# Kernel tuning notes

Hardware: AMD Instinct MI355X
Metric: run time of the kernel (lower is better)

Reference implementation:

```python
import jax, jax.numpy as jnp
import numpy as np

B, N, C = 2, 2048, 1024
H = 16
HD = C // H  # 64
SCALE = HD ** -0.5


def setup_inputs() -> dict:
    key = jax.random.key(0)
    ks = jax.random.split(key, 5)
    x = jax.random.normal(ks[0], (B, N, C), dtype=jnp.float32)
    # Linear params stored as [in, out] so y = x @ W + b (same math as torch x @ W.T + b)
    w_qkv = jax.random.normal(ks[1], (C, 3 * C), dtype=jnp.float32) * (C ** -0.5)
    b_qkv = jax.random.normal(ks[2], (3 * C,), dtype=jnp.float32) * 0.02
    w_proj = jax.random.normal(ks[3], (C, C), dtype=jnp.float32) * (C ** -0.5)
    b_proj = jax.random.normal(ks[4], (C,), dtype=jnp.float32) * 0.02
    return {"x": x, "w_qkv": w_qkv, "b_qkv": b_qkv, "w_proj": w_proj, "b_proj": b_proj}


def reference(x, w_qkv, b_qkv, w_proj, b_proj):
    # qkv projection: [B,N,3C] -> [3,B,H,N,HD]
    qkv = (x @ w_qkv + b_qkv).reshape(B, N, 3, H, HD)
    qkv = jnp.transpose(qkv, (2, 0, 3, 1, 4))
    q, k, v = qkv[0], qkv[1], qkv[2]
    # scaled dot-product attention, full [B,H,N,N] scores (faithful to source)
    attn = jnp.einsum('bhnd,bhmd->bhnm', q, k) * SCALE
    attn = jax.nn.softmax(attn, axis=-1)
    out = jnp.einsum('bhnm,bhmd->bhnd', attn, v)  # [B,H,N,HD]
    out = jnp.transpose(out, (0, 2, 1, 3)).reshape(B, N, C)
    return out @ w_proj + b_proj
```

## Files before the change

### kernel.cpp

```cpp
#include <hip/hip_runtime.h>


typedef __attribute__((ext_vector_type(4))) float f32x4;
typedef __attribute__((ext_vector_type(16))) float f32x16;
typedef __attribute__((ext_vector_type(8))) short bf16x8;
typedef __attribute__((ext_vector_type(8))) unsigned short u16x8;
typedef __attribute__((ext_vector_type(4))) unsigned short u16x4;
typedef __attribute__((ext_vector_type(2))) int i32x2;
typedef __attribute__((ext_vector_type(4))) int i32x4;

#define MFMA16 __builtin_amdgcn_mfma_f32_16x16x32_bf16
#define MFMA32 __builtin_amdgcn_mfma_f32_32x32x16_bf16
#define MEMFENCE asm volatile("" ::: "memory")
#define BARRIER() do { MEMFENCE; __builtin_amdgcn_s_barrier(); MEMFENCE; } while (0)

__device__ __forceinline__ unsigned short f2bf(float f) {
  unsigned int u = __float_as_uint(f);
  u += 0x7fffu + ((u >> 16) & 1u);
  return (unsigned short)(u >> 16);
}
__device__ __forceinline__ float bf2f(unsigned short h) {
  return __uint_as_float(((unsigned int)h) << 16);
}
__device__ __forceinline__ void gll16(const unsigned short* g, unsigned short* l) {
  __builtin_amdgcn_global_load_lds(
      (__attribute__((address_space(1))) void*)g,
      (__attribute__((address_space(3))) void*)l, 16, 0, 0);
}

__global__ __launch_bounds__(256) void prep_w_hi_kernel(
    const float* __restrict__ w, unsigned short* __restrict__ hi, int K, int N) {
  __shared__ float tile[64][65];
  const int k0 = blockIdx.x * 64, n0 = blockIdx.y * 64;
  const int tid = threadIdx.x;
  {
    const int r = tid >> 4, c = (tid & 15) * 4;
#pragma unroll
    for (int i = 0; i < 4; ++i) {
      const float4 v = *(const float4*)&w[(size_t)(k0 + r + i * 16) * N + n0 + c];
      tile[r + i * 16][c + 0] = v.x; tile[r + i * 16][c + 1] = v.y;
      tile[r + i * 16][c + 2] = v.z; tile[r + i * 16][c + 3] = v.w;
    }
  }
  __syncthreads();
  const int rn = tid >> 2, cb = (tid & 3) * 16;
  u16x8 h8[2];
#pragma unroll
  for (int j = 0; j < 16; ++j)
    h8[j >> 3][j & 7] = f2bf(tile[cb + j][rn]);
  const size_t o = (size_t)(n0 + rn) * K + k0 + cb;
  *(u16x8*)&hi[o] = h8[0]; *(u16x8*)&hi[o + 8] = h8[1];
}

__global__ __launch_bounds__(256) void cast_x_kernel(
    const float* __restrict__ x, unsigned short* __restrict__ hi) {
  const size_t i = ((size_t)blockIdx.x * 256 + threadIdx.x) * 4;
  const float4 v = *(const float4*)&x[i];
  u16x4 h;
  h[0] = f2bf(v.x); h[1] = f2bf(v.y); h[2] = f2bf(v.z); h[3] = f2bf(v.w);
  *(u16x4*)&hi[i] = h;
}

__global__ __launch_bounds__(256) void gemm_qkv_kernel(
    const unsigned short* __restrict__ Ahg, const unsigned short* __restrict__ Bhg,
    const float* __restrict__ bias,
    unsigned short* __restrict__ q_hi, unsigned short* __restrict__ k_hi,
    unsigned short* __restrict__ vt_hi) {
  __shared__ unsigned short Ah_s[3][128 * 32], Bh_s[3][128 * 32];
  const int tid = threadIdx.x;
  const int n0 = blockIdx.x * 128, m0 = blockIdx.y * 128;
  const int w = tid >> 6, lane = tid & 63;
  const int wm = (w >> 1) * 64, wn = (w & 1) * 64;
  const int lr = lane & 15, lg = lane >> 4;
  const int rr = lane >> 2, sl = lane & 3;
  const int r0 = w * 32 + rr;
  const int c0 = (sl ^ ((r0 >> 1) & 3)) * 8;
  const size_t a0 = (size_t)(m0 + r0) * 1024 + c0;
  const size_t a1 = (size_t)(m0 + r0 + 16) * 1024 + c0;
  const size_t b0 = (size_t)(n0 + r0) * 1024 + c0;
  const size_t b1 = (size_t)(n0 + r0 + 16) * 1024 + c0;
  const int wo = w * 1024;

#define GSTAGE(BUF, KO) do {                                          \
    gll16(&Ahg[a0 + (KO)], &Ah_s[BUF][wo]);                           \
    gll16(&Ahg[a1 + (KO)], &Ah_s[BUF][wo + 512]);                     \
    gll16(&Bhg[b0 + (KO)], &Bh_s[BUF][wo]);                           \
    gll16(&Bhg[b1 + (KO)], &Bh_s[BUF][wo + 512]);                     \
  } while (0)

  f32x4 acc[4][4] = {};
  GSTAGE(0, 0);
  GSTAGE(1, 32);
  int cur = 0;
  for (int t = 0; t < 32; ++t) {
    if (t < 31) asm volatile("s_waitcnt vmcnt(4)" ::: "memory");
    else        asm volatile("s_waitcnt vmcnt(0)" ::: "memory");
    __builtin_amdgcn_sched_barrier(0);
    BARRIER();
    if (t < 30) GSTAGE((cur + 2) % 3, (t + 2) * 32);
    bf16x8 afh[4], bfh[4];
#pragma unroll
    for (int i = 0; i < 4; ++i) {
      const int rA = wm + i * 16 + lr;
      const int oA = rA * 64 + ((lg * 16) ^ (((rA >> 1) & 3) << 4));
      afh[i] = *(const bf16x8*)((const char*)&Ah_s[cur][0] + oA);
      const int rB = wn + i * 16 + lr;
      const int oB = rB * 64 + ((lg * 16) ^ (((rB >> 1) & 3) << 4));
      bfh[i] = *(const bf16x8*)((const char*)&Bh_s[cur][0] + oB);
    }
#pragma unroll
    for (int i = 0; i < 4; ++i)
#pragma unroll
      for (int j = 0; j < 4; ++j)
        acc[i][j] = MFMA16(afh[i], bfh[j], acc[i][j], 0, 0, 0);
    cur = (cur + 1) % 3;
  }
#undef GSTAGE
#pragma unroll
  for (int j = 0; j < 4; ++j) {
    const int colg = n0 + wn + j * 16 + lr;
    const float bv = bias[colg];
    const int s = colg >> 10;
    const int c = colg & 1023;
    const int hh = c >> 6, d = c & 63;
    const float scl = (s == 0) ? 0.18033688011112042f : 1.0f;
#pragma unroll
    for (int i = 0; i < 4; ++i) {
      const int mg = m0 + wm + i * 16 + lg * 4;
      const int b = mg >> 11, nt = mg & 2047;
      if (s < 2) {
        unsigned short* dst = (s == 0) ? q_hi : k_hi;
        const size_t base = ((size_t)(b * 16 + hh) * 2048 + nt) * 64 + d;
#pragma unroll
        for (int r = 0; r < 4; ++r)
          dst[base + (size_t)r * 64] = f2bf((acc[i][j][r] + bv) * scl);
      } else {
        const size_t base = ((size_t)(b * 16 + hh) * 64 + d) * 2048 + nt;
        u16x4 hv;
#pragma unroll
        for (int r = 0; r < 4; ++r) hv[r] = f2bf(acc[i][j][r] + bv);
        *(u16x4*)&vt_hi[base] = hv;
      }
    }
  }
}

__global__ __launch_bounds__(256, 2) void attn_kernel(
    const unsigned short* __restrict__ q_hi, const unsigned short* __restrict__ k_hi,
    const unsigned short* __restrict__ vt_hi,
    unsigned short* __restrict__ ao_hi) {
  __shared__ unsigned short Kh_s[2][128 * 64];
  __shared__ unsigned short Vh_s[2][64 * 128];
  __shared__ float ls_s[4][32];
  const int tid = threadIdx.x;
  const int w = tid >> 6, lane = tid & 63;
  const int l31 = lane & 31, hi = lane >> 5;
  const int bid = blockIdx.x;
  const int bh = (bid & 7) * 4 + ((bid >> 3) & 3);
  const int qb = bid >> 5;
  const int qwave = qb * 128 + w * 32;

  bf16x8 qfh[4];
  {
    const size_t qrow = ((size_t)bh * 2048 + qwave + l31) * 64;
#pragma unroll
    for (int dc = 0; dc < 4; ++dc)
      qfh[dc] = *(const bf16x8*)&q_hi[qrow + dc * 16 + hi * 8];
  }

  const int krr = lane >> 3;
  const int kslot = (lane & 7) ^ krr;
  const int vrr = lane >> 4;
  const size_t kpan = (size_t)bh * 2048 * 64;
  const size_t vpan = (size_t)bh * 64 * 2048;

#define STAGE(BUF, T) do {                                                   \
    const int kvb_ = (T) * 128;                                              \
    _Pragma("unroll") for (int j = 0; j < 4; ++j) {                          \
      const int ch = 4 * w + j;                                              \
      gll16(&k_hi[kpan + (size_t)(kvb_ + ch * 8 + krr) * 64 + kslot * 8],    \
            &Kh_s[BUF][ch * 512]);                                           \
      const int vrow_ = ch * 4 + vrr;                                        \
      const int vslot_ = (lane & 15) ^ (vrow_ & 7);                          \
      gll16(&vt_hi[vpan + (size_t)vrow_ * 2048 + kvb_ + vslot_ * 8],         \
            &Vh_s[BUF][ch * 512]);                                           \
    } } while (0)

  f32x16 oacc[2] = {};
  float lsp = 0.f;

  STAGE(0, 0);
  int cur = 0;
  for (int t = 0; t < 16; ++t) {
    asm volatile("s_waitcnt vmcnt(0)" ::: "memory");
    __builtin_amdgcn_sched_barrier(0);
    BARRIER();
    if (t < 15) STAGE(cur ^ 1, t + 1);
    const char* Kb = (const char*)&Kh_s[cur][0];
    const char* Vb = (const char*)&Vh_s[cur][0];
#pragma unroll
    for (int s32 = 0; s32 < 4; ++s32) {
      f32x16 sv = {};
      const int krow = s32 * 32 + l31;
      const int kb = krow * 128;
      const int sx = (krow & 7) << 4;
#pragma unroll
      for (int dc = 0; dc < 4; ++dc) {
        const bf16x8 ah = *(const bf16x8*)(Kb + kb + ((dc * 32 + hi * 16) ^ sx));
        sv = MFMA32(ah, qfh[dc], sv, 0, 0, 0);
      }
      float p[16];
#pragma unroll
      for (int r = 0; r < 16; ++r) p[r] = __builtin_amdgcn_exp2f(sv[r]);
      lsp += ((p[0] + p[1]) + (p[2] + p[3])) + ((p[4] + p[5]) + (p[6] + p[7])) +
             (((p[8] + p[9]) + (p[10] + p[11])) + ((p[12] + p[13]) + (p[14] + p[15])));
      unsigned int W[8];
#pragma unroll
      for (int i = 0; i < 8; ++i)
        asm("v_cvt_pk_bf16_f32 %0, %1, %2" : "=v"(W[i]) : "v"(p[2 * i]), "v"(p[2 * i + 1]));
      const i32x2 s02 = __builtin_amdgcn_permlane32_swap((int)W[0], (int)W[2], false, false);
      const i32x2 s13 = __builtin_amdgcn_permlane32_swap((int)W[1], (int)W[3], false, false);
      const i32x2 s46 = __builtin_amdgcn_permlane32_swap((int)W[4], (int)W[6], false, false);
      const i32x2 s57 = __builtin_amdgcn_permlane32_swap((int)W[5], (int)W[7], false, false);
      union { i32x4 i; bf16x8 h; } pa0, pa1;
      pa0.i[0] = s02[0]; pa0.i[1] = s13[0]; pa0.i[2] = s02[1]; pa0.i[3] = s13[1];
      pa1.i[0] = s46[0]; pa1.i[1] = s57[0]; pa1.i[2] = s46[1]; pa1.i[3] = s57[1];
#pragma unroll
      for (int dc = 0; dc < 2; ++dc) {
        const int vrow = dc * 32 + l31;
        const int vb = vrow * 256;
        const int vsx = (vrow & 7) << 4;
#pragma unroll
        for (int kc = 0; kc < 2; ++kc) {
          const int off = (s32 * 64 + kc * 32 + hi * 16) ^ vsx;
          const bf16x8 vh = *(const bf16x8*)(Vb + vb + off);
          const bf16x8 pf = kc ? pa1.h : pa0.h;
          oacc[dc] = MFMA32(pf, vh, oacc[dc], 0, 0, 0);
        }
      }
    }
    cur ^= 1;
  }
#undef STAGE

  {
    const i32x2 sw = __builtin_amdgcn_permlane32_swap(
        __float_as_int(lsp), __float_as_int(lsp), false, false);
    const float lst = __int_as_float(sw[0]) + __int_as_float(sw[1]);
    if (lane < 32) ls_s[w][lane] = lst;
  }
  asm volatile("s_waitcnt lgkmcnt(0)" ::: "memory");
  __builtin_amdgcn_sched_barrier(0);

  const int b = bh >> 4, hh = bh & 15;
#pragma unroll
  for (int r = 0; r < 16; ++r) {
    const int qr = (r & 3) + 8 * (r >> 2) + 4 * hi;
    const float inv = 1.0f / ls_s[w][qr];
    const size_t rowa = ((size_t)b * 2048 + qwave + qr) * 1024 + hh * 64 + l31;
#pragma unroll
    for (int dc = 0; dc < 2; ++dc)
      ao_hi[rowa + dc * 32] = f2bf(oacc[dc][r] * inv);
  }
}

__global__ __launch_bounds__(256) void gemm_proj_kernel(
    const unsigned short* __restrict__ Ahg, const unsigned short* __restrict__ Bhg,
    const float* __restrict__ bias, float* __restrict__ out) {
  __shared__ unsigned short Ah_s[3][64 * 32], Bh_s[3][128 * 32];
  const int tid = threadIdx.x;
  const int n0 = blockIdx.x * 128, m0 = blockIdx.y * 64;
  const int w = tid >> 6, lane = tid & 63;
  const int wm = (w >> 1) * 32, wn = (w & 1) * 64;
  const int lr = lane & 15, lg = lane >> 4;
  const int rla = lane >> 2, sl = lane & 3;
  const int rowA = w * 16 + rla;
  const int colA = (sl ^ ((rowA >> 1) & 3)) * 8;
  const size_t aoff = (size_t)(m0 + rowA) * 1024 + colA;
  const int rowB = w * 32 + rla;
  const int colB = (sl ^ ((rowB >> 1) & 3)) * 8;
  const size_t boff0 = (size_t)(n0 + rowB) * 1024 + colB;
  const size_t boff1 = boff0 + (size_t)16 * 1024;
  const int adst = w * 512, bdst = w * 1024;

#define GSTAGE(BUF, KO) do {                                          \
    gll16(&Ahg[aoff + (KO)], &Ah_s[BUF][adst]);                       \
    gll16(&Bhg[boff0 + (KO)], &Bh_s[BUF][bdst]);                      \
    gll16(&Bhg[boff1 + (KO)], &Bh_s[BUF][bdst + 512]);                \
  } while (0)

  f32x4 acc[2][4] = {};
  GSTAGE(0, 0);
  GSTAGE(1, 32);
  int cur = 0;
  for (int t = 0; t < 32; ++t) {
    if (t < 31) asm volatile("s_waitcnt vmcnt(3)" ::: "memory");
    else        asm volatile("s_waitcnt vmcnt(0)" ::: "memory");
    __builtin_amdgcn_sched_barrier(0);
    BARRIER();
    if (t < 30) GSTAGE((cur + 2) % 3, (t + 2) * 32);
    bf16x8 afh[2], bfh[4];
#pragma unroll
    for (int i = 0; i < 2; ++i) {
      const int rA = wm + i * 16 + lr;
      const int oA = rA * 64 + ((lg * 16) ^ (((rA >> 1) & 3) << 4));
      afh[i] = *(const bf16x8*)((const char*)&Ah_s[cur][0] + oA);
    }
#pragma unroll
    for (int j = 0; j < 4; ++j) {
      const int rB = wn + j * 16 + lr;
      const int oB = rB * 64 + ((lg * 16) ^ (((rB >> 1) & 3) << 4));
      bfh[j] = *(const bf16x8*)((const char*)&Bh_s[cur][0] + oB);
    }
#pragma unroll
    for (int i = 0; i < 2; ++i)
#pragma unroll
      for (int j = 0; j < 4; ++j)
        acc[i][j] = MFMA16(afh[i], bfh[j], acc[i][j], 0, 0, 0);
    cur = (cur + 1) % 3;
  }
#undef GSTAGE
#pragma unroll
  for (int j = 0; j < 4; ++j) {
    const int colg = n0 + wn + j * 16 + lr;
    const float bv = bias[colg];
#pragma unroll
    for (int i = 0; i < 2; ++i) {
      const int mg = m0 + wm + i * 16 + lg * 4;
#pragma unroll
      for (int r = 0; r < 4; ++r)
        out[(size_t)(mg + r) * 1024 + colg] = acc[i][j][r] + bv;
    }
  }
}

extern "C" void kernel_launch(void* const* d_in, const int* in_sizes, int n_in,
                              void* d_out, int out_size, void* d_ws, size_t ws_size,
                              hipStream_t stream) {
  const float* x = (const float*)d_in[0];
  const float* w_qkv = (const float*)d_in[1];
  const float* b_qkv = (const float*)d_in[2];
  const float* w_proj = (const float*)d_in[3];
  const float* b_proj = (const float*)d_in[4];
  float* out = (float*)d_out;

  char* ws = (char*)d_ws;
  size_t off = 0;
  auto alloc = [&](size_t elems) -> unsigned short* {
    unsigned short* p = (unsigned short*)(ws + off);
    off += ((elems * 2) + 255) & ~(size_t)255;
    return p;
  };
  unsigned short* xh  = alloc(4096 * 1024);
  unsigned short* wqh = alloc(3072 * 1024);
  unsigned short* wph = alloc(1024 * 1024);
  unsigned short* qh  = alloc((size_t)32 * 2048 * 64);
  unsigned short* kh  = alloc((size_t)32 * 2048 * 64);
  unsigned short* vth = alloc((size_t)32 * 64 * 2048);
  unsigned short* aoh = alloc(4096 * 1024);
  if (off > ws_size) return;

  prep_w_hi_kernel<<<dim3(16, 48), 256, 0, stream>>>(w_qkv, wqh, 1024, 3072);
  prep_w_hi_kernel<<<dim3(16, 16), 256, 0, stream>>>(w_proj, wph, 1024, 1024);
  cast_x_kernel<<<4096, 256, 0, stream>>>(x, xh);
  gemm_qkv_kernel<<<dim3(24, 32), 256, 0, stream>>>(xh, wqh, b_qkv, qh, kh, vth);
  attn_kernel<<<512, 256, 0, stream>>>(qh, kh, vth, aoh);
  gemm_proj_kernel<<<dim3(8, 64), 256, 0, stream>>>(aoh, wph, b_proj, out);
}
```

Measured before the change: 112.6 us.

## Process two query groups per wave and compute row sums via MFMA

Each wave now handles 64 query rows (two 32-row groups) instead of 32. The K and V fragments loaded from LDS are reused across both groups, which halves LDS traffic per unit of work, and the grid shrinks to 256 blocks. The softmax denominator is now accumulated with an MFMA against a ones vector, using bf16-rounded probabilities, instead of scalar fp32 adds plus a permlane/LDS reduction. The cost is more registers per wave, which may hurt occupancy under launch bounds of 2, and with 256 blocks on 256 CUs there is less latency hiding.

```diff
diff --git a/kernel.cpp b/kernel.cpp
--- a/kernel.cpp
+++ b/kernel.cpp
@@ -151,21 +151,21 @@
     unsigned short* __restrict__ ao_hi) {
   __shared__ unsigned short Kh_s[2][128 * 64];
   __shared__ unsigned short Vh_s[2][64 * 128];
-  __shared__ float ls_s[4][32];
   const int tid = threadIdx.x;
   const int w = tid >> 6, lane = tid & 63;
   const int l31 = lane & 31, hi = lane >> 5;
   const int bid = blockIdx.x;
   const int bh = (bid & 7) * 4 + ((bid >> 3) & 3);
   const int qb = bid >> 5;
-  const int qwave = qb * 128 + w * 32;
-
-  bf16x8 qfh[4];
-  {
-    const size_t qrow = ((size_t)bh * 2048 + qwave + l31) * 64;
+  const int qwave = qb * 256 + w * 64;
+
+  bf16x8 qf[2][4];
+#pragma unroll
+  for (int g = 0; g < 2; ++g) {
+    const size_t qrow = ((size_t)bh * 2048 + qwave + g * 32 + l31) * 64;
 #pragma unroll
     for (int dc = 0; dc < 4; ++dc)
-      qfh[dc] = *(const bf16x8*)&q_hi[qrow + dc * 16 + hi * 8];
+      qf[g][dc] = *(const bf16x8*)&q_hi[qrow + dc * 16 + hi * 8];
   }
 
   const int krr = lane >> 3;
@@ -186,8 +186,11 @@
             &Vh_s[BUF][ch * 512]);                                           \
     } } while (0)
 
-  f32x16 oacc[2] = {};
-  float lsp = 0.f;
+  f32x16 oacc[2][2] = {};
+  f32x16 lsacc[2] = {};
+  bf16x8 ones;
+#pragma unroll
+  for (int j = 0; j < 8; ++j) ones[j] = (short)0x3F80;
 
   STAGE(0, 0);
   int cur = 0;
@@ -200,42 +203,49 @@
     const char* Vb = (const char*)&Vh_s[cur][0];
 #pragma unroll
     for (int s32 = 0; s32 < 4; ++s32) {
-      f32x16 sv = {};
       const int krow = s32 * 32 + l31;
       const int kb = krow * 128;
       const int sx = (krow & 7) << 4;
-#pragma unroll
-      for (int dc = 0; dc < 4; ++dc) {
-        const bf16x8 ah = *(const bf16x8*)(Kb + kb + ((dc * 32 + hi * 16) ^ sx));
-        sv = MFMA32(ah, qfh[dc], sv, 0, 0, 0);
-      }
-      float p[16];
-#pragma unroll
-      for (int r = 0; r < 16; ++r) p[r] = __builtin_amdgcn_exp2f(sv[r]);
-      lsp += ((p[0] + p[1]) + (p[2] + p[3])) + ((p[4] + p[5]) + (p[6] + p[7])) +
-             (((p[8] + p[9]) + (p[10] + p[11])) + ((p[12] + p[13]) + (p[14] + p[15])));
-      unsigned int W[8];
-#pragma unroll
-      for (int i = 0; i < 8; ++i)
-        asm("v_cvt_pk_bf16_f32 %0, %1, %2" : "=v"(W[i]) : "v"(p[2 * i]), "v"(p[2 * i + 1]));
-      const i32x2 s02 = __builtin_amdgcn_permlane32_swap((int)W[0], (int)W[2], false, false);
-      const i32x2 s13 = __builtin_amdgcn_permlane32_swap((int)W[1], (int)W[3], false, false);
-      const i32x2 s46 = __builtin_amdgcn_permlane32_swap((int)W[4], (int)W[6], false, false);
-      const i32x2 s57 = __builtin_amdgcn_permlane32_swap((int)W[5], (int)W[7], false, false);
-      union { i32x4 i; bf16x8 h; } pa0, pa1;
-      pa0.i[0] = s02[0]; pa0.i[1] = s13[0]; pa0.i[2] = s02[1]; pa0.i[3] = s13[1];
-      pa1.i[0] = s46[0]; pa1.i[1] = s57[0]; pa1.i[2] = s46[1]; pa1.i[3] = s57[1];
+      bf16x8 ah[4];
+#pragma unroll
+      for (int dc = 0; dc < 4; ++dc)
+        ah[dc] = *(const bf16x8*)(Kb + kb + ((dc * 32 + hi * 16) ^ sx));
+      bf16x8 vh[2][2];
 #pragma unroll
       for (int dc = 0; dc < 2; ++dc) {
         const int vrow = dc * 32 + l31;
         const int vb = vrow * 256;
         const int vsx = (vrow & 7) << 4;
 #pragma unroll
-        for (int kc = 0; kc < 2; ++kc) {
-          const int off = (s32 * 64 + kc * 32 + hi * 16) ^ vsx;
-          const bf16x8 vh = *(const bf16x8*)(Vb + vb + off);
-          const bf16x8 pf = kc ? pa1.h : pa0.h;
-          oacc[dc] = MFMA32(pf, vh, oacc[dc], 0, 0, 0);
+        for (int kc = 0; kc < 2; ++kc)
+          vh[dc][kc] = *(const bf16x8*)(Vb + vb + ((s32 * 64 + kc * 32 + hi * 16) ^ vsx));
+      }
+#pragma unroll
+      for (int g = 0; g < 2; ++g) {
+        f32x16 sv = {};
+#pragma unroll
+        for (int dc = 0; dc < 4; ++dc)
+          sv = MFMA32(ah[dc], qf[g][dc], sv, 0, 0, 0);
+        float p[16];
+#pragma unroll
+        for (int r = 0; r < 16; ++r) p[r] = __builtin_amdgcn_exp2f(sv[r]);
+        unsigned int W[8];
+#pragma unroll
+        for (int i = 0; i < 8; ++i)
+          asm("v_cvt_pk_bf16_f32 %0, %1, %2" : "=v"(W[i]) : "v"(p[2 * i]), "v"(p[2 * i + 1]));
+        const i32x2 s02 = __builtin_amdgcn_permlane32_swap((int)W[0], (int)W[2], false, false);
+        const i32x2 s13 = __builtin_amdgcn_permlane32_swap((int)W[1], (int)W[3], false, false);
+        const i32x2 s46 = __builtin_amdgcn_permlane32_swap((int)W[4], (int)W[6], false, false);
+        const i32x2 s57 = __builtin_amdgcn_permlane32_swap((int)W[5], (int)W[7], false, false);
+        union { i32x4 i; bf16x8 h; } pa0, pa1;
+        pa0.i[0] = s02[0]; pa0.i[1] = s13[0]; pa0.i[2] = s02[1]; pa0.i[3] = s13[1];
+        pa1.i[0] = s46[0]; pa1.i[1] = s57[0]; pa1.i[2] = s46[1]; pa1.i[3] = s57[1];
+        lsacc[g] = MFMA32(pa0.h, ones, lsacc[g], 0, 0, 0);
+        lsacc[g] = MFMA32(pa1.h, ones, lsacc[g], 0, 0, 0);
+#pragma unroll
+        for (int dc = 0; dc < 2; ++dc) {
+          oacc[g][dc] = MFMA32(pa0.h, vh[dc][0], oacc[g][dc], 0, 0, 0);
+          oacc[g][dc] = MFMA32(pa1.h, vh[dc][1], oacc[g][dc], 0, 0, 0);
         }
       }
     }
@@ -243,25 +253,19 @@
   }
 #undef STAGE
 
-  {
-    const i32x2 sw = __builtin_amdgcn_permlane32_swap(
-        __float_as_int(lsp), __float_as_int(lsp), false, false);
-    const float lst = __int_as_float(sw[0]) + __int_as_float(sw[1]);
-    if (lane < 32) ls_s[w][lane] = lst;
-  }
-  asm volatile("s_waitcnt lgkmcnt(0)" ::: "memory");
-  __builtin_amdgcn_sched_barrier(0);
-
   const int b = bh >> 4, hh = bh & 15;
 #pragma unroll
-  for (int r = 0; r < 16; ++r) {
-    const int qr = (r & 3) + 8 * (r >> 2) + 4 * hi;
-    const float inv = 1.0f / ls_s[w][qr];
-    const size_t rowa = ((size_t)b * 2048 + qwave + qr) * 1024 + hh * 64 + l31;
-#pragma unroll
-    for (int dc = 0; dc < 2; ++dc)
-      ao_hi[rowa + dc * 32] = f2bf(oacc[dc][r] * inv);
-  }
+  for (int g = 0; g < 2; ++g)
+#pragma unroll
+    for (int r = 0; r < 16; ++r) {
+      const int qr = (r & 3) + 8 * (r >> 2) + 4 * hi;
+      const float inv = 1.0f / lsacc[g][r];
+      const size_t rowa =
+          ((size_t)b * 2048 + qwave + g * 32 + qr) * 1024 + hh * 64 + l31;
+#pragma unroll
+      for (int dc = 0; dc < 2; ++dc)
+        ao_hi[rowa + dc * 32] = f2bf(oacc[g][dc][r] * inv);
+    }
 }
 
 __global__ __launch_bounds__(256) void gemm_proj_kernel(
@@ -364,6 +368,6 @@
   prep_w_hi_kernel<<<dim3(16, 16), 256, 0, stream>>>(w_proj, wph, 1024, 1024);
   cast_x_kernel<<<4096, 256, 0, stream>>>(x, xh);
   gemm_qkv_kernel<<<dim3(24, 32), 256, 0, stream>>>(xh, wqh, b_qkv, qh, kh, vth);
-  attn_kernel<<<512, 256, 0, stream>>>(qh, kh, vth, aoh);
+  attn_kernel<<<256, 256, 0, stream>>>(qh, kh, vth, aoh);
   gemm_proj_kernel<<<dim3(8, 64), 256, 0, stream>>>(aoh, wph, b_proj, out);
 }
```

Measured after the change: 116.8 us. 1.04x slower.

## Double attention block to 8 waves and compute row sums via MFMA with ones

Applied to the files above, without the earlier changes.

The attention kernel now launches 256 blocks of 512 threads, with each block covering 256 query rows. Each K/V tile staged into shared memory is therefore reused by twice as many waves, and each wave issues half as many global-to-LDS loads. The softmax denominator is no longer a scalar add tree plus a permlane reduction through shared memory. Instead it is accumulated by two extra MFMAs of the bf16 probabilities against a vector of ones, so each lane holds the row sums directly in output layout. This trades VALU adds for extra matrix-core work and rounds P to bf16 before summing. It also drops the launch_bounds occupancy hint of 2 blocks and grows accumulator register pressure.

```diff
diff --git a/kernel.cpp b/kernel.cpp
--- a/kernel.cpp
+++ b/kernel.cpp
@@ -145,27 +145,26 @@
   }
 }
 
-__global__ __launch_bounds__(256, 2) void attn_kernel(
+__global__ __launch_bounds__(512) void attn_kernel(
     const unsigned short* __restrict__ q_hi, const unsigned short* __restrict__ k_hi,
     const unsigned short* __restrict__ vt_hi,
     unsigned short* __restrict__ ao_hi) {
   __shared__ unsigned short Kh_s[2][128 * 64];
   __shared__ unsigned short Vh_s[2][64 * 128];
-  __shared__ float ls_s[4][32];
   const int tid = threadIdx.x;
-  const int w = tid >> 6, lane = tid & 63;
+  const int wq = tid >> 6, lane = tid & 63;
   const int l31 = lane & 31, hi = lane >> 5;
   const int bid = blockIdx.x;
   const int bh = (bid & 7) * 4 + ((bid >> 3) & 3);
   const int qb = bid >> 5;
-  const int qwave = qb * 128 + w * 32;
-
-  bf16x8 qfh[4];
+  const int qwave = qb * 256 + wq * 32;
+
+  bf16x8 qf[4];
   {
     const size_t qrow = ((size_t)bh * 2048 + qwave + l31) * 64;
 #pragma unroll
     for (int dc = 0; dc < 4; ++dc)
-      qfh[dc] = *(const bf16x8*)&q_hi[qrow + dc * 16 + hi * 8];
+      qf[dc] = *(const bf16x8*)&q_hi[qrow + dc * 16 + hi * 8];
   }
 
   const int krr = lane >> 3;
@@ -176,8 +175,8 @@
 
 #define STAGE(BUF, T) do {                                                   \
     const int kvb_ = (T) * 128;                                              \
-    _Pragma("unroll") for (int j = 0; j < 4; ++j) {                          \
-      const int ch = 4 * w + j;                                              \
+    _Pragma("unroll") for (int j = 0; j < 2; ++j) {                          \
+      const int ch = 2 * wq + j;                                             \
       gll16(&k_hi[kpan + (size_t)(kvb_ + ch * 8 + krr) * 64 + kslot * 8],    \
             &Kh_s[BUF][ch * 512]);                                           \
       const int vrow_ = ch * 4 + vrr;                                        \
@@ -187,7 +186,10 @@
     } } while (0)
 
   f32x16 oacc[2] = {};
-  float lsp = 0.f;
+  f32x16 lsacc = {};
+  bf16x8 ones;
+#pragma unroll
+  for (int j = 0; j < 8; ++j) ones[j] = (short)0x3F80;
 
   STAGE(0, 0);
   int cur = 0;
@@ -207,13 +209,11 @@
 #pragma unroll
       for (int dc = 0; dc < 4; ++dc) {
         const bf16x8 ah = *(const bf16x8*)(Kb + kb + ((dc * 32 + hi * 16) ^ sx));
-        sv = MFMA32(ah, qfh[dc], sv, 0, 0, 0);
+        sv = MFMA32(ah, qf[dc], sv, 0, 0, 0);
       }
       float p[16];
 #pragma unroll
       for (int r = 0; r < 16; ++r) p[r] = __builtin_amdgcn_exp2f(sv[r]);
-      lsp += ((p[0] + p[1]) + (p[2] + p[3])) + ((p[4] + p[5]) + (p[6] + p[7])) +
-             (((p[8] + p[9]) + (p[10] + p[11])) + ((p[12] + p[13]) + (p[14] + p[15])));
       unsigned int W[8];
 #pragma unroll
       for (int i = 0; i < 8; ++i)
@@ -225,38 +225,28 @@
       union { i32x4 i; bf16x8 h; } pa0, pa1;
       pa0.i[0] = s02[0]; pa0.i[1] = s13[0]; pa0.i[2] = s02[1]; pa0.i[3] = s13[1];
       pa1.i[0] = s46[0]; pa1.i[1] = s57[0]; pa1.i[2] = s46[1]; pa1.i[3] = s57[1];
+      lsacc = MFMA32(pa0.h, ones, lsacc, 0, 0, 0);
+      lsacc = MFMA32(pa1.h, ones, lsacc, 0, 0, 0);
 #pragma unroll
       for (int dc = 0; dc < 2; ++dc) {
         const int vrow = dc * 32 + l31;
         const int vb = vrow * 256;
         const int vsx = (vrow & 7) << 4;
-#pragma unroll
-        for (int kc = 0; kc < 2; ++kc) {
-          const int off = (s32 * 64 + kc * 32 + hi * 16) ^ vsx;
-          const bf16x8 vh = *(const bf16x8*)(Vb + vb + off);
-          const bf16x8 pf = kc ? pa1.h : pa0.h;
-          oacc[dc] = MFMA32(pf, vh, oacc[dc], 0, 0, 0);
-        }
+        const bf16x8 vh0 = *(const bf16x8*)(Vb + vb + ((s32 * 64 + hi * 16) ^ vsx));
+        const bf16x8 vh1 = *(const bf16x8*)(Vb + vb + ((s32 * 64 + 32 + hi * 16) ^ vsx));
+        oacc[dc] = MFMA32(pa0.h, vh0, oacc[dc], 0, 0, 0);
+        oacc[dc] = MFMA32(pa1.h, vh1, oacc[dc], 0, 0, 0);
       }
     }
     cur ^= 1;
   }
 #undef STAGE
-
-  {
-    const i32x2 sw = __builtin_amdgcn_permlane32_swap(
-        __float_as_int(lsp), __float_as_int(lsp), false, false);
-    const float lst = __int_as_float(sw[0]) + __int_as_float(sw[1]);
-    if (lane < 32) ls_s[w][lane] = lst;
-  }
-  asm volatile("s_waitcnt lgkmcnt(0)" ::: "memory");
-  __builtin_amdgcn_sched_barrier(0);
 
   const int b = bh >> 4, hh = bh & 15;
 #pragma unroll
   for (int r = 0; r < 16; ++r) {
     const int qr = (r & 3) + 8 * (r >> 2) + 4 * hi;
-    const float inv = 1.0f / ls_s[w][qr];
+    const float inv = 1.0f / lsacc[r];
     const size_t rowa = ((size_t)b * 2048 + qwave + qr) * 1024 + hh * 64 + l31;
 #pragma unroll
     for (int dc = 0; dc < 2; ++dc)
@@ -364,6 +354,6 @@
   prep_w_hi_kernel<<<dim3(16, 16), 256, 0, stream>>>(w_proj, wph, 1024, 1024);
   cast_x_kernel<<<4096, 256, 0, stream>>>(x, xh);
   gemm_qkv_kernel<<<dim3(24, 32), 256, 0, stream>>>(xh, wqh, b_qkv, qh, kh, vth);
-  attn_kernel<<<512, 256, 0, stream>>>(qh, kh, vth, aoh);
+  attn_kernel<<<256, 512, 0, stream>>>(qh, kh, vth, aoh);
   gemm_proj_kernel<<<dim3(8, 64), 256, 0, stream>>>(aoh, wph, b_proj, out);
 }
```

After: 114.1 us. About the same (+1.4%).
